# Kernel tuning notes

Measured on AMD Instinct MI355X. Metric: run time of the kernel, lower is better.

The kernel has to match this reference:

```python
import jax, jax.numpy as jnp
import numpy as np
from jax import lax

B, C1, C2, OUT, H, W = 8, 256, 128, 256, 64, 64
MID = max(C1, C2)
D = max(MID // 8, 4)

def conv1x1(x, w, b=None):
    # x: [B,C,H,W], w: [O,C]
    y = jnp.einsum('bchw,oc->bohw', x, w)
    if b is not None:
        y = y + b[None, :, None, None]
    return y

def dwconv3x3(x, w, b):
    # depthwise 3x3, padding=1; w: [C,1,3,3]
    y = lax.conv_general_dilated(x, w, (1, 1), 'SAME',
                                 dimension_numbers=('NCHW', 'OIHW', 'NCHW'),
                                 feature_group_count=x.shape[1])
    return y + b[None, :, None, None]

def setup_inputs() -> dict:
    key = jax.random.key(0)
    ks = jax.random.split(key, 16)
    def w1x1(k, o, i):
        return jax.random.normal(k, (o, i), jnp.float32) * np.sqrt(2.0 / o)
    def wdw(k, c):
        return jax.random.normal(k, (c, 1, 3, 3), jnp.float32) * np.sqrt(2.0 / (9 * c))
    z = lambda c: jnp.zeros((c,), jnp.float32)
    return {
        'x1': jax.random.normal(ks[0], (B, C1, H, W), jnp.float32),
        'x2': jax.random.normal(ks[1], (B, C2, H, W), jnp.float32),
        'conv_r_w': w1x1(ks[2], MID, C1), 'conv_r_b': z(MID),
        'conv_n_w': w1x1(ks[3], MID, C2), 'conv_n_b': z(MID),
        'mlp_w1': w1x1(ks[4], D, MID),
        'mlp_w2': w1x1(ks[5], 2 * MID, D),
        'pq_w': w1x1(ks[6], MID, MID), 'pq_b': z(MID),
        'dq_w': wdw(ks[7], MID), 'dq_b': z(MID),
        'pk_w': w1x1(ks[8], MID, MID), 'pk_b': z(MID),
        'dk_w': wdw(ks[9], MID), 'dk_b': z(MID),
        'pv_w': w1x1(ks[10], MID, MID), 'pv_b': z(MID),
        'dv_w': wdw(ks[11], MID), 'dv_b': z(MID),
        'out_w': w1x1(ks[12], OUT, MID), 'out_b': z(OUT),
        'alpha': jnp.float32(1.0),
        'lambd': jnp.float32(0.5),
        'beta': jnp.float32(0.5),
    }

def reference(x1, x2, conv_r_w, conv_r_b, conv_n_w, conv_n_b, mlp_w1, mlp_w2,
              pq_w, pq_b, dq_w, dq_b, pk_w, pk_b, dk_w, dk_b,
              pv_w, pv_b, dv_w, dv_b, out_w, out_b, alpha, lambd, beta):
    FR = conv1x1(x1, conv_r_w, conv_r_b)          # [B,C,H,W]
    FN = conv1x1(x2, conv_n_w, conv_n_b)          # [B,C,H,W]
    stack = jnp.stack([FR, FN], axis=1)           # [B,2,C,H,W]
    feats_sum = FR + FN
    pooled = feats_sum.mean(axis=(2, 3))          # [B,C] (adaptive avg pool 1x1)
    h = jax.nn.relu(jnp.einsum('bc,dc->bd', pooled, mlp_w1))
    a = jnp.einsum('bd,ed->be', h, mlp_w2).reshape(B, 2, MID)
    attn = jax.nn.softmax(a, axis=1)              # softmax over the 2 branches
    Fw = jnp.einsum('bkchw,bkc->bchw', stack, attn)
    Q = dwconv3x3(conv1x1(Fw, pq_w, pq_b), dq_w, dq_b)
    K = dwconv3x3(conv1x1(Fw, pk_w, pk_b), dk_w, dk_b)
    V = dwconv3x3(conv1x1(Fw, pv_w, pv_b), dv_w, dv_b)
    FQ = jnp.fft.fft2(Q.astype(jnp.float32), axes=(-2, -1))   # complex64 [B,C,H,W]
    FK = jnp.fft.fft2(K.astype(jnp.float32), axes=(-2, -1))
    elem = (FQ * FK).reshape(B, MID, H * W)                    # [B,C,HW]
    FQf = FQ.reshape(B, MID, H * W)
    FKf = FK.reshape(B, MID, H * W)
    attn_matrix = jnp.einsum('bcn,bdn->bcd', FQf, FKf)         # complex [B,C,C]
    attn_w = jax.nn.softmax(jnp.abs(attn_matrix) / alpha, axis=-1)
    attn_wc = attn_w.astype(jnp.complex64)
    F_CFR = jnp.einsum('bcd,bdn->bcn', attn_wc, elem).reshape(B, MID, H, W)
    cfr = jnp.real(jnp.fft.ifft2(F_CFR, axes=(-2, -1))).astype(Q.dtype)
    F_DFR = V - lambd * V * cfr
    freq_out = Q * cfr + F_DFR
    output = beta * freq_out + (1.0 - beta) * Fw
    return conv1x1(output, out_w, out_b)
```

## Files before the change

### kernel.cpp

```cpp
#include <hip/hip_runtime.h>
#include <math.h>

#ifndef M_PI
#define M_PI 3.14159265358979323846
#endif

typedef unsigned int u32;

constexpr int  NB   = 8;
constexpr int  CH   = 256;
constexpr long HW   = 4096;
constexpr long SLOT = (long)NB * CH * HW;
constexpr int  SPLITK = 8;
constexpr long ST   = (long)CH * HW;

__device__ __forceinline__ float rne_hi(float x) {
  unsigned u = __float_as_uint(x);
  unsigned r = (u + 0x7FFFu + ((u >> 16) & 1u)) & 0xFFFF0000u;
  return __uint_as_float(r);
}
__device__ __forceinline__ u32 packf(float x) {
  const float h = rne_hi(x);
  const float l = x - h;
  return (__float_as_uint(h) & 0xFFFF0000u) | (__float_as_uint(l) >> 16);
}
__device__ __forceinline__ float unpackf(u32 u) {
  return __uint_as_float(u & 0xFFFF0000u) + __uint_as_float(u << 16);
}
__device__ __forceinline__ unsigned bfpair(float x, float y) {
  return (__float_as_uint(x) >> 16) | (__float_as_uint(y) & 0xFFFF0000u);
}

typedef short bf16x8 __attribute__((ext_vector_type(8)));
typedef float f32x4  __attribute__((ext_vector_type(4)));

struct CvtJob { const float* src; u32* dst; int n4; };

__global__ __launch_bounds__(256)
void cvt_kernel(CvtJob j0, CvtJob j1, CvtJob j2, CvtJob j3, CvtJob j4, CvtJob j5)
{
  const int yy = blockIdx.y;
  CvtJob j;
  switch (yy) {
    case 0: j = j0; break;
    case 1: j = j1; break;
    case 2: j = j2; break;
    case 3: j = j3; break;
    case 4: j = j4; break;
    default: j = j5; break;
  }
  const int i = blockIdx.x * 256 + threadIdx.x;
  if (i < j.n4) {
    const float4 v = ((const float4*)j.src)[i];
    uint4 o;
    o.x = packf(v.x); o.y = packf(v.y); o.z = packf(v.z); o.w = packf(v.w);
    ((uint4*)j.dst)[i] = o;
  }
}

struct GemmSet {
  const u32*   A;
  const void*  B;
  void*        C;
  const float* bias;
  int          K;
  long         bStride;
};

#define SWZ(row, chunk) (((row) << 5) + ((((chunk) ^ ((row) & 3))) << 3))

template<bool BPACKED, int EPI>
__global__ __launch_bounds__(512, 2)
void gemm_mfma(GemmSet g0, GemmSet g1, GemmSet g2,
               long aStride, long cStride,
               const u32* __restrict__ qb, const u32* __restrict__ vb,
               const u32* __restrict__ fwb,
               const float* __restrict__ lambd, const float* __restrict__ beta)
{
  constexpr int N = 4096;
  __shared__ __align__(16) unsigned short sAh[256 * 32];
  __shared__ __align__(16) unsigned short sAl[256 * 32];
  __shared__ __align__(16) unsigned short sBh[128 * 32];
  __shared__ __align__(16) unsigned short sBl[128 * 32];

  const int tid = threadIdx.x;
  const int b   = blockIdx.z;
  const int yy  = blockIdx.y;
  const int n0  = blockIdx.x * 128;

  const GemmSet g = (yy == 0) ? g0 : ((yy == 1) ? g1 : g2);
  const u32*   A       = g.A;
  const void*  Bv      = g.B;
  void*        Cv      = g.C;
  const float* bias    = g.bias;
  const int    K       = g.K;
  const long   bStride = g.bStride;

  const u32* Ab = A + (long)b * aStride;

  const int ar = tid >> 1;
  const int ak = (tid & 1) * 16;
  const int ac0 = (tid & 1) * 2;
  const int bn = tid & 127;
  const int bc0 = tid >> 7;
  const int bk = bc0 * 8;

  const int wv = tid >> 6, lane = tid & 63;
  const int wy = wv >> 1, wx = wv & 1;
  const int quad = lane >> 4, l15 = lane & 15;

  f32x4 acc[4][4];
#pragma unroll
  for (int i = 0; i < 4; ++i)
#pragma unroll
    for (int j = 0; j < 4; ++j) acc[i][j] = (f32x4){0.f, 0.f, 0.f, 0.f};

  u32   ra[16];
  u32   rbu[8];
  float rbf[8];
  {
    const u32* ap = Ab + (long)ar * K + ak;
#pragma unroll
    for (int i = 0; i < 4; ++i) {
      const uint4 t = *(const uint4*)(ap + i * 4);
      ra[4*i] = t.x; ra[4*i+1] = t.y; ra[4*i+2] = t.z; ra[4*i+3] = t.w;
    }
    if (BPACKED) {
      const u32* bp = (const u32*)Bv + (long)b * bStride + (long)bk * N + n0 + bn;
#pragma unroll
      for (int i = 0; i < 8; ++i) rbu[i] = bp[(long)i * N];
    } else {
      const float* bp = (const float*)Bv + (long)b * bStride + (long)bk * N + n0 + bn;
#pragma unroll
      for (int i = 0; i < 8; ++i) rbf[i] = bp[(long)i * N];
    }
  }

  for (int kt = 0; kt < K; kt += 32) {
    {
      u32 hi[8], lo[8];
#pragma unroll
      for (int e = 0; e < 8; ++e) {
        const u32 u0 = ra[2*e], u1 = ra[2*e+1];
        hi[e] = (u0 >> 16) | (u1 & 0xFFFF0000u);
        lo[e] = (u0 & 0xFFFFu) | (u1 << 16);
      }
      *(uint4*)&sAh[SWZ(ar, ac0)]     = make_uint4(hi[0], hi[1], hi[2], hi[3]);
      *(uint4*)&sAh[SWZ(ar, ac0 + 1)] = make_uint4(hi[4], hi[5], hi[6], hi[7]);
      *(uint4*)&sAl[SWZ(ar, ac0)]     = make_uint4(lo[0], lo[1], lo[2], lo[3]);
      *(uint4*)&sAl[SWZ(ar, ac0 + 1)] = make_uint4(lo[4], lo[5], lo[6], lo[7]);
    }
    if (BPACKED) {
      u32 hi[4], lo[4];
#pragma unroll
      for (int e = 0; e < 4; ++e) {
        const u32 u0 = rbu[2*e], u1 = rbu[2*e+1];
        hi[e] = (u0 >> 16) | (u1 & 0xFFFF0000u);
        lo[e] = (u0 & 0xFFFFu) | (u1 << 16);
      }
      *(uint4*)&sBh[SWZ(bn, bc0)] = make_uint4(hi[0], hi[1], hi[2], hi[3]);
      *(uint4*)&sBl[SWZ(bn, bc0)] = make_uint4(lo[0], lo[1], lo[2], lo[3]);
    } else {
      float h[8], l[8];
#pragma unroll
      for (int e = 0; e < 8; ++e) { h[e] = rne_hi(rbf[e]); l[e] = rbf[e] - h[e]; }
      *(uint4*)&sBh[SWZ(bn, bc0)] = make_uint4(bfpair(h[0],h[1]), bfpair(h[2],h[3]),
                                               bfpair(h[4],h[5]), bfpair(h[6],h[7]));
      *(uint4*)&sBl[SWZ(bn, bc0)] = make_uint4(bfpair(l[0],l[1]), bfpair(l[2],l[3]),
                                               bfpair(l[4],l[5]), bfpair(l[6],l[7]));
    }
    __syncthreads();

    if (kt + 32 < K) {
      const u32* ap = Ab + (long)ar * K + kt + 32 + ak;
#pragma unroll
      for (int i = 0; i < 4; ++i) {
        const uint4 t = *(const uint4*)(ap + i * 4);
        ra[4*i] = t.x; ra[4*i+1] = t.y; ra[4*i+2] = t.z; ra[4*i+3] = t.w;
      }
      if (BPACKED) {
        const u32* bp = (const u32*)Bv + (long)b * bStride + (long)(kt + 32 + bk) * N + n0 + bn;
#pragma unroll
        for (int i = 0; i < 8; ++i) rbu[i] = bp[(long)i * N];
      } else {
        const float* bp = (const float*)Bv + (long)b * bStride + (long)(kt + 32 + bk) * N + n0 + bn;
#pragma unroll
        for (int i = 0; i < 8; ++i) rbf[i] = bp[(long)i * N];
      }
    }

    bf16x8 ah[4], al[4];
#pragma unroll
    for (int i = 0; i < 4; ++i) {
      const int rowa = wy * 64 + i * 16 + l15;
      ah[i] = *(const bf16x8*)&sAh[SWZ(rowa, quad)];
      al[i] = *(const bf16x8*)&sAl[SWZ(rowa, quad)];
    }
#pragma unroll
    for (int j = 0; j < 4; ++j) {
      const int rowb = wx * 64 + j * 16 + l15;
      const bf16x8 bh = *(const bf16x8*)&sBh[SWZ(rowb, quad)];
      const bf16x8 bl = *(const bf16x8*)&sBl[SWZ(rowb, quad)];
#pragma unroll
      for (int i = 0; i < 4; ++i) {
        acc[i][j] = __builtin_amdgcn_mfma_f32_16x16x32_bf16(ah[i], bh, acc[i][j], 0, 0, 0);
        acc[i][j] = __builtin_amdgcn_mfma_f32_16x16x32_bf16(ah[i], bl, acc[i][j], 0, 0, 0);
        acc[i][j] = __builtin_amdgcn_mfma_f32_16x16x32_bf16(al[i], bh, acc[i][j], 0, 0, 0);
      }
    }
    __syncthreads();
  }

  if (EPI == 0) {
    float* Cb = (float*)Cv + (long)b * cStride;
#pragma unroll
    for (int i = 0; i < 4; ++i)
#pragma unroll
      for (int r = 0; r < 4; ++r) {
        const int row = wy * 64 + i * 16 + quad * 4 + r;
        const float bb = bias ? bias[row] : 0.f;
#pragma unroll
        for (int j = 0; j < 4; ++j) {
          const int col = n0 + wx * 64 + j * 16 + l15;
          Cb[(long)row * N + col] = acc[i][j][r] + bb;
        }
      }
  } else if (EPI == 1) {
    u32* Cb = (u32*)Cv + (long)b * cStride;
#pragma unroll
    for (int i = 0; i < 4; ++i)
#pragma unroll
      for (int r = 0; r < 4; ++r) {
        const int row = wy * 64 + i * 16 + quad * 4 + r;
        const float bb = bias ? bias[row] : 0.f;
#pragma unroll
        for (int j = 0; j < 4; ++j) {
          const int col = n0 + wx * 64 + j * 16 + l15;
          Cb[(long)row * N + col] = packf(acc[i][j][r] + bb);
        }
      }
  } else {
    u32* Cb = (u32*)Cv + (long)b * cStride;
    const float lam = lambd[0], bet = beta[0];
#pragma unroll
    for (int i = 0; i < 4; ++i)
#pragma unroll
      for (int r = 0; r < 4; ++r) {
        const int row = wy * 64 + i * 16 + quad * 4 + r;
#pragma unroll
        for (int j = 0; j < 4; ++j) {
          const int col = n0 + wx * 64 + j * 16 + l15;
          const long off = (long)row * N + col;
          const long gi  = (long)b * cStride + off;
          const float q = unpackf(qb[gi]);
          const float v = unpackf(vb[gi]);
          const float f = unpackf(fwb[gi]);
          Cb[off] = packf(bet * (acc[i][j][r] * (q - lam * v) + v) + (1.f - bet) * f);
        }
      }
  }
}

__global__ __launch_bounds__(256)
void gemm_logits(const u32* __restrict__ Q, const u32* __restrict__ Kr,
                 float* __restrict__ Lp)
{
  __shared__ __align__(16) unsigned short sAh[128 * 48];
  __shared__ __align__(16) unsigned short sAl[128 * 48];
  __shared__ __align__(16) unsigned short sBh[128 * 48];
  __shared__ __align__(16) unsigned short sBl[128 * 48];

  const int tid = threadIdx.x;
  const int bz  = blockIdx.z;
  const int b   = bz >> 3, sp = bz & 7;
  const int m0  = blockIdx.y * 128;
  const int n0  = blockIdx.x * 128;
  const long k0b = (long)sp * 512;

  const int ar = tid >> 1;
  const int ak = (tid & 1) * 16;
  const int aBase = ar * 48 + ak;

  const int wv = tid >> 6, lane = tid & 63;
  const int wy = wv >> 1, wx = wv & 1;
  const int quad = lane >> 4, l15 = lane & 15;

  f32x4 acc[4][4];
#pragma unroll
  for (int i = 0; i < 4; ++i)
#pragma unroll
    for (int j = 0; j < 4; ++j) acc[i][j] = (f32x4){0.f, 0.f, 0.f, 0.f};

  const u32* Abase = Q  + (long)b * ST + (long)(m0 + ar) * 4096 + k0b + ak;
  const u32* Bbase = Kr + (long)b * ST + (long)(n0 + ar) * 4096 + k0b + ak;

  u32 ra[16], rb[16];
#pragma unroll
  for (int i = 0; i < 4; ++i) {
    uint4 t = *(const uint4*)(Abase + i * 4);
    ra[4*i] = t.x; ra[4*i+1] = t.y; ra[4*i+2] = t.z; ra[4*i+3] = t.w;
    t = *(const uint4*)(Bbase + i * 4);
    rb[4*i] = t.x; rb[4*i+1] = t.y; rb[4*i+2] = t.z; rb[4*i+3] = t.w;
  }

  for (int kt = 0; kt < 512; kt += 32) {
    {
      u32 hi[8], lo[8];
#pragma unroll
      for (int e = 0; e < 8; ++e) {
        const u32 u0 = ra[2*e], u1 = ra[2*e+1];
        hi[e] = (u0 >> 16) | (u1 & 0xFFFF0000u);
        lo[e] = (u0 & 0xFFFFu) | (u1 << 16);
      }
      *(uint4*)&sAh[aBase]     = make_uint4(hi[0], hi[1], hi[2], hi[3]);
      *(uint4*)&sAh[aBase + 8] = make_uint4(hi[4], hi[5], hi[6], hi[7]);
      *(uint4*)&sAl[aBase]     = make_uint4(lo[0], lo[1], lo[2], lo[3]);
      *(uint4*)&sAl[aBase + 8] = make_uint4(lo[4], lo[5], lo[6], lo[7]);
#pragma unroll
      for (int e = 0; e < 8; ++e) {
        const u32 u0 = rb[2*e], u1 = rb[2*e+1];
        hi[e] = (u0 >> 16) | (u1 & 0xFFFF0000u);
        lo[e] = (u0 & 0xFFFFu) | (u1 << 16);
      }
      *(uint4*)&sBh[aBase]     = make_uint4(hi[0], hi[1], hi[2], hi[3]);
      *(uint4*)&sBh[aBase + 8] = make_uint4(hi[4], hi[5], hi[6], hi[7]);
      *(uint4*)&sBl[aBase]     = make_uint4(lo[0], lo[1], lo[2], lo[3]);
      *(uint4*)&sBl[aBase + 8] = make_uint4(lo[4], lo[5], lo[6], lo[7]);
    }
    __syncthreads();

    if (kt + 32 < 512) {
#pragma unroll
      for (int i = 0; i < 4; ++i) {
        uint4 t = *(const uint4*)(Abase + kt + 32 + i * 4);
        ra[4*i] = t.x; ra[4*i+1] = t.y; ra[4*i+2] = t.z; ra[4*i+3] = t.w;
        t = *(const uint4*)(Bbase + kt + 32 + i * 4);
        rb[4*i] = t.x; rb[4*i+1] = t.y; rb[4*i+2] = t.z; rb[4*i+3] = t.w;
      }
    }

    bf16x8 ah[4], al[4];
#pragma unroll
    for (int i = 0; i < 4; ++i) {
      const int idx = (wy * 64 + i * 16 + l15) * 48 + quad * 8;
      ah[i] = *(const bf16x8*)&sAh[idx];
      al[i] = *(const bf16x8*)&sAl[idx];
    }
#pragma unroll
    for (int j = 0; j < 4; ++j) {
      const int idx = (wx * 64 + j * 16 + l15) * 48 + quad * 8;
      const bf16x8 bh = *(const bf16x8*)&sBh[idx];
      const bf16x8 bl = *(const bf16x8*)&sBl[idx];
#pragma unroll
      for (int i = 0; i < 4; ++i) {
        acc[i][j] = __builtin_amdgcn_mfma_f32_16x16x32_bf16(ah[i], bh, acc[i][j], 0, 0, 0);
        acc[i][j] = __builtin_amdgcn_mfma_f32_16x16x32_bf16(ah[i], bl, acc[i][j], 0, 0, 0);
        acc[i][j] = __builtin_amdgcn_mfma_f32_16x16x32_bf16(al[i], bh, acc[i][j], 0, 0, 0);
      }
    }
    __syncthreads();
  }

  float* Lb = Lp + (long)bz * 65536;
#pragma unroll
  for (int i = 0; i < 4; ++i)
#pragma unroll
    for (int r = 0; r < 4; ++r) {
      const int row = m0 + wy * 64 + i * 16 + quad * 4 + r;
#pragma unroll
      for (int j = 0; j < 4; ++j) {
        const int col = n0 + wx * 64 + j * 16 + l15;
        Lb[(long)row * 256 + col] = acc[i][j][r];
      }
    }
}

__global__ __launch_bounds__(256)
void pool_kernel(const u32* __restrict__ FR, const u32* __restrict__ FN,
                 float* __restrict__ pooled)
{
  __shared__ float red[256];
  const int bc = blockIdx.x, tid = threadIdx.x;
  const uint4* a = (const uint4*)(FR + (long)bc * HW);
  const uint4* b = (const uint4*)(FN + (long)bc * HW);
  float s = 0.f;
  for (int v = tid; v < 1024; v += 256) {
    const uint4 x = a[v];
    s += unpackf(x.x) + unpackf(x.y) + unpackf(x.z) + unpackf(x.w);
    const uint4 y = b[v];
    s += unpackf(y.x) + unpackf(y.y) + unpackf(y.z) + unpackf(y.w);
  }
  red[tid] = s; __syncthreads();
  for (int o = 128; o > 0; o >>= 1) {
    if (tid < o) red[tid] += red[tid + o];
    __syncthreads();
  }
  if (tid == 0) pooled[bc] = red[0] * (1.f / 4096.f);
}

__global__ __launch_bounds__(256)
void attn2_kernel(const float* __restrict__ pooled, const float* __restrict__ w1,
                  const float* __restrict__ w2, float* __restrict__ attn2)
{
  __shared__ float ps[256];
  __shared__ float hs[32];
  const int b = blockIdx.x, tid = threadIdx.x;
  ps[tid] = pooled[b * 256 + tid];
  __syncthreads();
  if (tid < 32) {
    float a = 0.f;
    for (int c = 0; c < 256; ++c) a += ps[c] * w1[tid * 256 + c];
    hs[tid] = fmaxf(a, 0.f);
  }
  __syncthreads();
  float a0 = 0.f, a1 = 0.f;
  for (int d = 0; d < 32; ++d) {
    const float h = hs[d];
    a0 += h * w2[tid * 32 + d];
    a1 += h * w2[(256 + tid) * 32 + d];
  }
  const float m  = fmaxf(a0, a1);
  const float e0 = expf(a0 - m), e1 = expf(a1 - m);
  const float inv = 1.f / (e0 + e1);
  attn2[b * 512 + tid]       = e0 * inv;
  attn2[b * 512 + 256 + tid] = e1 * inv;
}

__global__ __launch_bounds__(256)
void fw_kernel(const u32* __restrict__ FR, const u32* __restrict__ FN,
               const float* __restrict__ attn2, u32* __restrict__ FW)
{
  const int b = blockIdx.z, c = blockIdx.y;
  const float a0 = attn2[b * 512 + c];
  const float a1 = attn2[b * 512 + 256 + c];
  const long base4 = ((long)b * 256 + c) * 1024;
  const int i = blockIdx.x * 256 + threadIdx.x;
  const uint4 r = ((const uint4*)FR)[base4 + i];
  const uint4 n = ((const uint4*)FN)[base4 + i];
  uint4 o;
  o.x = packf(a0 * unpackf(r.x) + a1 * unpackf(n.x));
  o.y = packf(a0 * unpackf(r.y) + a1 * unpackf(n.y));
  o.z = packf(a0 * unpackf(r.z) + a1 * unpackf(n.z));
  o.w = packf(a0 * unpackf(r.w) + a1 * unpackf(n.w));
  ((uint4*)FW)[base4 + i] = o;
}

struct DwJob { const u32* in; const float* w; const float* bias; u32* out; u32* out_rev; };

__global__ __launch_bounds__(256)
void dw_kernel(DwJob j0, DwJob j1, DwJob j2)
{
  __shared__ float img[66][66];
  const int yy = blockIdx.y;
  const DwJob j = (yy == 0) ? j0 : ((yy == 1) ? j1 : j2);
  const int bc = blockIdx.x, tid = threadIdx.x;
  const int c = bc & 255;
  for (int v = tid; v < 66 * 66; v += 256) ((float*)img)[v] = 0.f;
  __syncthreads();
  const uint4* in4 = (const uint4*)(j.in + (long)bc * HW);
  for (int v = tid; v < 1024; v += 256) {
    const uint4 x = in4[v];
    const int r = v >> 4, c0 = ((v & 15) << 2) + 1;
    img[r + 1][c0 + 0] = unpackf(x.x);
    img[r + 1][c0 + 1] = unpackf(x.y);
    img[r + 1][c0 + 2] = unpackf(x.z);
    img[r + 1][c0 + 3] = unpackf(x.w);
  }
  float wr[9];
#pragma unroll
  for (int jj = 0; jj < 9; ++jj) wr[jj] = j.w[c * 9 + jj];
  const float bb = j.bias[c];
  __syncthreads();
  for (int p = tid; p < 4096; p += 256) {
    const int y = p >> 6, x = p & 63;
    float s = bb;
#pragma unroll
    for (int ky = 0; ky < 3; ++ky)
#pragma unroll
      for (int kx = 0; kx < 3; ++kx)
        s = fmaf(wr[ky * 3 + kx], img[y + ky][x + kx], s);
    const u32 u = packf(s);
    j.out[(long)bc * HW + p] = u;
    if (j.out_rev)
      j.out_rev[(long)bc * HW + (((64 - y) & 63) << 6) + ((64 - x) & 63)] = u;
  }
}

#define SWA(r, c) (((r) << 6) | ((c) ^ (r)))
#define REV6(x)   ((((x) & 3) << 4) | ((x) & 12) | ((x) >> 4))

__device__ __forceinline__ float2 cmul(float2 a, float2 w) {
  return make_float2(a.x * w.x - a.y * w.y, a.x * w.y + a.y * w.x);
}
__device__ __forceinline__ float2 cmulc(float2 a, float2 w) {
  return make_float2(a.x * w.x + a.y * w.y, a.y * w.x - a.x * w.y);
}
__device__ __forceinline__ void r4fwd(float2& x0, float2& x1, float2& x2, float2& x3) {
  const float2 t0 = make_float2(x0.x + x2.x, x0.y + x2.y);
  const float2 t1 = make_float2(x0.x - x2.x, x0.y - x2.y);
  const float2 t2 = make_float2(x1.x + x3.x, x1.y + x3.y);
  const float2 t3 = make_float2(x1.x - x3.x, x1.y - x3.y);
  x0 = make_float2(t0.x + t2.x, t0.y + t2.y);
  x2 = make_float2(t0.x - t2.x, t0.y - t2.y);
  x1 = make_float2(t1.x + t3.y, t1.y - t3.x);
  x3 = make_float2(t1.x - t3.y, t1.y + t3.x);
}
__device__ __forceinline__ void r4inv(float2& x0, float2& x1, float2& x2, float2& x3) {
  const float2 t0 = make_float2(x0.x + x2.x, x0.y + x2.y);
  const float2 t1 = make_float2(x0.x - x2.x, x0.y - x2.y);
  const float2 t2 = make_float2(x1.x + x3.x, x1.y + x3.y);
  const float2 t3 = make_float2(x1.x - x3.x, x1.y - x3.y);
  x0 = make_float2(t0.x + t2.x, t0.y + t2.y);
  x2 = make_float2(t0.x - t2.x, t0.y - t2.y);
  x1 = make_float2(t1.x - t3.y, t1.y + t3.x);
  x3 = make_float2(t1.x + t3.y, t1.y - t3.x);
}

__device__ __forceinline__ void fused01_fwd(float2* __restrict__ Z,
                                            const float2 (&wA)[3][3],
                                            int lane, int kb, int pass)
{
  float2 x[16];
#pragma unroll
  for (int m = 0; m < 16; ++m) {
    const int p = 16 * kb + m;
    x[m] = Z[pass ? SWA(p, lane) : SWA(lane, p)];
  }
#pragma unroll
  for (int c = 0; c < 4; ++c)
    r4fwd(x[4*c], x[4*c+1], x[4*c+2], x[4*c+3]);
#pragma unroll
  for (int j = 0; j < 4; ++j) {
    if (j) {
      x[j+4]  = cmul(x[j+4],  wA[j-1][0]);
      x[j+8]  = cmul(x[j+8],  wA[j-1][1]);
      x[j+12] = cmul(x[j+12], wA[j-1][2]);
    }
    r4fwd(x[j], x[j+4], x[j+8], x[j+12]);
  }
#pragma unroll
  for (int m = 0; m < 16; ++m) {
    const int p = 16 * kb + m;
    Z[pass ? SWA(p, lane) : SWA(lane, p)] = x[m];
  }
}

__device__ __forceinline__ void stage2_fwd(float2* __restrict__ Z,
                                           const float2 (&wB)[4][3],
                                           int lane, int kb, int pass)
{
#pragma unroll
  for (int q = 0; q < 4; ++q) {
    const int k = kb + 4 * q;
    const int a0 = pass ? SWA(k,      lane) : SWA(lane, k);
    const int a1 = pass ? SWA(k + 16, lane) : SWA(lane, k + 16);
    const int a2 = pass ? SWA(k + 32, lane) : SWA(lane, k + 32);
    const int a3 = pass ? SWA(k + 48, lane) : SWA(lane, k + 48);
    float2 x0 = Z[a0], x1 = Z[a1], x2 = Z[a2], x3 = Z[a3];
    x1 = cmul(x1, wB[q][0]);
    x2 = cmul(x2, wB[q][1]);
    x3 = cmul(x3, wB[q][2]);
    r4fwd(x0, x1, x2, x3);
    Z[a0] = x0; Z[a1] = x1; Z[a2] = x2; Z[a3] = x3;
  }
}

__device__ __forceinline__ void stage2_inv(float2* __restrict__ Z,
                                           const float2 (&wB)[4][3],
                                           int lane, int kb, int pass)
{
#pragma unroll
  for (int q = 0; q < 4; ++q) {
    const int k = kb + 4 * q;
    const int a0 = pass ? SWA(lane, k)      : SWA(k,      lane);
    const int a1 = pass ? SWA(lane, k + 16) : SWA(k + 16, lane);
    const int a2 = pass ? SWA(lane, k + 32) : SWA(k + 32, lane);
    const int a3 = pass ? SWA(lane, k + 48) : SWA(k + 48, lane);
    float2 x0 = Z[a0], x1 = Z[a1], x2 = Z[a2], x3 = Z[a3];
    r4inv(x0, x1, x2, x3);
    x1 = cmulc(x1, wB[q][0]);
    x2 = cmulc(x2, wB[q][1]);
    x3 = cmulc(x3, wB[q][2]);
    Z[a0] = x0; Z[a1] = x1; Z[a2] = x2; Z[a3] = x3;
  }
}

__device__ __forceinline__ void fused01_inv(float2* __restrict__ Z,
                                            const float2 (&wA)[3][3],
                                            int lane, int kb, int pass)
{
  float2 x[16];
#pragma unroll
  for (int m = 0; m < 16; ++m) {
    const int p = 16 * kb + m;
    x[m] = Z[pass ? SWA(lane, p) : SWA(p, lane)];
  }
#pragma unroll
  for (int j = 0; j < 4; ++j) {
    r4inv(x[j], x[j+4], x[j+8], x[j+12]);
    if (j) {
      x[j+4]  = cmulc(x[j+4],  wA[j-1][0]);
      x[j+8]  = cmulc(x[j+8],  wA[j-1][1]);
      x[j+12] = cmulc(x[j+12], wA[j-1][2]);
    }
  }
#pragma unroll
  for (int c = 0; c < 4; ++c)
    r4inv(x[4*c], x[4*c+1], x[4*c+2], x[4*c+3]);
#pragma unroll
  for (int m = 0; m < 16; ++m) {
    const int p = 16 * kb + m;
    Z[pass ? SWA(lane, p) : SWA(p, lane)] = x[m];
  }
}

__device__ __forceinline__ void sconv_load(float2* __restrict__ Z,
                                           const u32* __restrict__ Qg,
                                           const u32* __restrict__ Kg,
                                           long base, int tid)
{
  const uint4* Q4 = (const uint4*)(Qg + base);
  const uint4* K4 = (const uint4*)(Kg + base);
#pragma unroll
  for (int i = 0; i < 4; ++i) {
    const int v = tid + 256 * i;
    const uint4 q = Q4[v], k = K4[v];
    const int r = v >> 4, w = v & 15;
    const int R  = REV6(r);
    const int cb = ((w & 3) << 2) | (w >> 2);
    Z[SWA(R, cb)]      = make_float2(unpackf(q.x), unpackf(k.x));
    Z[SWA(R, cb + 16)] = make_float2(unpackf(q.y), unpackf(k.y));
    Z[SWA(R, cb + 32)] = make_float2(unpackf(q.z), unpackf(k.z));
    Z[SWA(R, cb + 48)] = make_float2(unpackf(q.w), unpackf(k.w));
  }
}

__global__ __launch_bounds__(256, 2)
void sconv_kernel(const u32* __restrict__ Qg, const u32* __restrict__ Kg,
                  u32* __restrict__ Sg)
{
  __shared__ float2 ZA[4096];
  __shared__ float2 ZB[4096];
  const int tid  = threadIdx.x;
  const int lane = tid & 63;
  const int kb   = tid >> 6;
  const long base = (long)blockIdx.x * 8192;

  const float2 wA[3][3] = {
    { make_float2( 0.92387953251f, -0.38268343236f),
      make_float2( 0.70710678119f, -0.70710678119f),
      make_float2( 0.38268343236f, -0.92387953251f) },
    { make_float2( 0.70710678119f, -0.70710678119f),
      make_float2( 0.f,            -1.f),
      make_float2(-0.70710678119f, -0.70710678119f) },
    { make_float2( 0.38268343236f, -0.92387953251f),
      make_float2(-0.70710678119f, -0.70710678119f),
      make_float2(-0.92387953251f,  0.38268343236f) } };
  float2 wB[4][3];
#pragma unroll
  for (int q = 0; q < 4; ++q) {
    const float k = (float)(kb + 4 * q);
    float sn, cs;
    __sincosf(-2.f * (float)M_PI * (1.f / 64.f) * k,        &sn, &cs); wB[q][0] = make_float2(cs, sn);
    __sincosf(-2.f * (float)M_PI * (1.f / 64.f) * (2.f*k),  &sn, &cs); wB[q][1] = make_float2(cs, sn);
    __sincosf(-2.f * (float)M_PI * (1.f / 64.f) * (3.f*k),  &sn, &cs); wB[q][2] = make_float2(cs, sn);
  }

  sconv_load(ZA, Qg, Kg, base, tid);
  sconv_load(ZB, Qg, Kg, base + 4096, tid);
  __syncthreads();

  for (int pass = 0; pass < 2; ++pass) {
    fused01_fwd(ZA, wA, lane, kb, pass);
    fused01_fwd(ZB, wA, lane, kb, pass);
    __syncthreads();
    stage2_fwd(ZA, wB, lane, kb, pass);
    stage2_fwd(ZB, wB, lane, kb, pass);
    __syncthreads();
  }

#pragma unroll
  for (int i = 0; i < 9; ++i) {
    const int n = tid + 256 * i;
    if (n < 2112) {
      const int u = n >> 6, vv = n & 63;
      if (!((u == 0 || u == 32) && vv > 32)) {
        const int u2 = (64 - u) & 63, v2 = (64 - vv) & 63;
        const int az = SWA(u, vv), am = SWA(u2, v2);
        const float2 z0 = ZA[az], m0 = ZA[am];
        const float2 z1 = ZB[az], m1 = ZB[am];
        const float dre0 = 0.25f * (z0.x*z0.x - z0.y*z0.y - m0.x*m0.x + m0.y*m0.y);
        const float dim0 = 0.5f  * (z0.x*z0.y + m0.x*m0.y);
        const float dre1 = 0.25f * (z1.x*z1.x - z1.y*z1.y - m1.x*m1.x + m1.y*m1.y);
        const float dim1 = 0.5f  * (z1.x*z1.y + m1.x*m1.y);
        ZA[az] = make_float2(dim0 + dre1, dim1 - dre0);
        ZA[am] = make_float2(dim0 - dre1, dim1 + dre0);
      }
    }
  }
  __syncthreads();

  for (int pass = 0; pass < 2; ++pass) {
    stage2_inv(ZA, wB, lane, kb, pass);
    __syncthreads();
    fused01_inv(ZA, wA, lane, kb, pass);
    __syncthreads();
  }

  uint4* Sa = (uint4*)(Sg + base);
  uint4* Sb = (uint4*)(Sg + base + 4096);
#pragma unroll
  for (int i = 0; i < 4; ++i) {
    const int v = tid + 256 * i;
    const int y = v >> 4, w = v & 15;
    const int Rr = REV6(y);
    const int cb = ((w & 3) << 2) | (w >> 2);
    const float2 e0 = ZA[SWA(Rr, cb)];
    const float2 e1 = ZA[SWA(Rr, cb + 16)];
    const float2 e2 = ZA[SWA(Rr, cb + 32)];
    const float2 e3 = ZA[SWA(Rr, cb + 48)];
    uint4 o;
    o.x = packf(e0.x * (1.f / 4096.f));
    o.y = packf(e1.x * (1.f / 4096.f));
    o.z = packf(e2.x * (1.f / 4096.f));
    o.w = packf(e3.x * (1.f / 4096.f));
    Sa[v] = o;
    o.x = packf(e0.y * (1.f / 4096.f));
    o.y = packf(e1.y * (1.f / 4096.f));
    o.z = packf(e2.y * (1.f / 4096.f));
    o.w = packf(e3.y * (1.f / 4096.f));
    Sb[v] = o;
  }
}

__global__ __launch_bounds__(256)
void softmax_kernel(const float* __restrict__ Lp, u32* __restrict__ L,
                    const float* __restrict__ alpha)
{
  __shared__ float red[256];
  const int row = blockIdx.x, tid = threadIdx.x;
  const int b = row >> 8, c = row & 255;
  const float sc = 4096.f / alpha[0];
  float acc = 0.f;
#pragma unroll
  for (int s = 0; s < SPLITK; ++s)
    acc += Lp[((long)(b * SPLITK + s) * 65536) + (long)c * 256 + tid];
  const float v = fabsf(acc) * sc;
  red[tid] = v; __syncthreads();
  for (int o = 128; o > 0; o >>= 1) {
    if (tid < o) red[tid] = fmaxf(red[tid], red[tid + o]);
    __syncthreads();
  }
  const float mx = red[0];
  __syncthreads();
  const float e = expf(v - mx);
  red[tid] = e; __syncthreads();
  for (int o = 128; o > 0; o >>= 1) {
    if (tid < o) red[tid] += red[tid + o];
    __syncthreads();
  }
  L[(long)row * 256 + tid] = packf(e / red[0]);
}

extern "C" void kernel_launch(void* const* d_in, const int* in_sizes, int n_in,
                              void* d_out, int out_size, void* d_ws, size_t ws_size,
                              hipStream_t stream)
{
  const float* x1       = (const float*)d_in[0];
  const float* x2       = (const float*)d_in[1];
  const float* conv_r_w = (const float*)d_in[2];
  const float* conv_r_b = (const float*)d_in[3];
  const float* conv_n_w = (const float*)d_in[4];
  const float* conv_n_b = (const float*)d_in[5];
  const float* mlp_w1   = (const float*)d_in[6];
  const float* mlp_w2   = (const float*)d_in[7];
  const float* pq_w     = (const float*)d_in[8];
  const float* pq_b     = (const float*)d_in[9];
  const float* dq_w     = (const float*)d_in[10];
  const float* dq_b     = (const float*)d_in[11];
  const float* pk_w     = (const float*)d_in[12];
  const float* pk_b     = (const float*)d_in[13];
  const float* dk_w     = (const float*)d_in[14];
  const float* dk_b     = (const float*)d_in[15];
  const float* pv_w     = (const float*)d_in[16];
  const float* pv_b     = (const float*)d_in[17];
  const float* dv_w     = (const float*)d_in[18];
  const float* dv_b     = (const float*)d_in[19];
  const float* out_w    = (const float*)d_in[20];
  const float* out_b    = (const float*)d_in[21];
  const float* alpha    = (const float*)d_in[22];
  const float* lambd    = (const float*)d_in[23];
  const float* beta     = (const float*)d_in[24];

  u32* s = (u32*)d_ws;
  u32* S0 = s;
  u32* S1 = s + SLOT;
  u32* S2 = s + 2 * SLOT;
  u32* S3 = s + 3 * SLOT;
  u32* S4 = s + 4 * SLOT;
  u32* S5 = s + 5 * SLOT;
  float* Lp     = (float*)(s + 6 * SLOT);
  u32*   Lb     = (u32*)(Lp + (long)8 * SPLITK * 65536);
  float* pooled = (float*)(Lb + (long)8 * 65536);
  float* attn2  = pooled + 2048;
  u32*   wR     = (u32*)(attn2 + 4096);
  u32*   wN     = wR + 65536;
  u32*   wQ     = wN + 32768;
  u32*   wK     = wQ + 65536;
  u32*   wV     = wK + 65536;
  u32*   wO     = wV + 65536;

  const size_t needed =
      (size_t)(6 * SLOT + (long)8 * SPLITK * 65536 + 8L * 65536 + 2048 + 4096
               + 65536 * 5 + 32768) * 4;
  if (ws_size < needed) return;

  const long ST2 = (long)128 * HW;
  const long STL = (long)256 * 256;

  {
    CvtJob jR{conv_r_w, wR, 16384};
    CvtJob jQ{pq_w,     wQ, 16384};
    CvtJob jK{pk_w,     wK, 16384};
    CvtJob jV{pv_w,     wV, 16384};
    CvtJob jO{out_w,    wO, 16384};
    CvtJob jN{conv_n_w, wN, 8192};
    cvt_kernel<<<dim3(64, 6), 256, 0, stream>>>(jR, jQ, jK, jV, jO, jN);
  }

  {
    GemmSet gR{wR, (const void*)x1, (void*)S0, conv_r_b, 256, ST};
    GemmSet gN{wN, (const void*)x2, (void*)S1, conv_n_b, 128, ST2};
    gemm_mfma<false, 1><<<dim3(32, 2, 8), 512, 0, stream>>>(gR, gN, gN,
        0L, ST, nullptr, nullptr, nullptr, nullptr, nullptr);
  }

  pool_kernel<<<2048, 256, 0, stream>>>(S0, S1, pooled);
  attn2_kernel<<<8, 256, 0, stream>>>(pooled, mlp_w1, mlp_w2, attn2);
  fw_kernel<<<dim3(4, 256, 8), 256, 0, stream>>>(S0, S1, attn2, S2);

  {
    GemmSet gQ{wQ, (const void*)S2, (void*)S3, pq_b, 256, ST};
    GemmSet gK{wK, (const void*)S2, (void*)S4, pk_b, 256, ST};
    GemmSet gV{wV, (const void*)S2, (void*)S5, pv_b, 256, ST};
    gemm_mfma<true, 1><<<dim3(32, 3, 8), 512, 0, stream>>>(gQ, gK, gV,
        0L, ST, nullptr, nullptr, nullptr, nullptr, nullptr);
  }

  {
    DwJob jQ{S3, dq_w, dq_b, S0, nullptr};
    DwJob jK{S4, dk_w, dk_b, S1, S3};
    DwJob jV{S5, dv_w, dv_b, S4, nullptr};
    dw_kernel<<<dim3(2048, 3), 256, 0, stream>>>(jQ, jK, jV);
  }

  sconv_kernel<<<1024, 256, 0, stream>>>(S0, S1, S5);

  gemm_logits<<<dim3(2, 2, 64), 256, 0, stream>>>(S0, S3, Lp);
  softmax_kernel<<<2048, 256, 0, stream>>>(Lp, Lb, alpha);

  {
    GemmSet gM{Lb, (const void*)S5, (void*)S2, nullptr, 256, ST};
    gemm_mfma<true, 2><<<dim3(32, 1, 8), 512, 0, stream>>>(gM, gM, gM,
        STL, ST, S0, S4, S2, lambd, beta);
  }

  {
    GemmSet gO{wO, (const void*)S2, d_out, out_b, 256, ST};
    gemm_mfma<true, 0><<<dim3(32, 1, 8), 512, 0, stream>>>(gO, gO, gO,
        0L, ST, nullptr, nullptr, nullptr, nullptr, nullptr);
  }
}
```

Baseline: 440.8 us.

## Double-buffer GEMM shared tiles with padded rows instead of XOR swizzle

Converts the MFMA GEMM's LDS staging to a two-buffer ping-pong so the next tile is committed after the MFMA work and only one barrier per k-step is needed. The XOR swizzle is replaced by a padded row stride of 48 elements. This raises LDS use to about 144KB per block, which likely drops residency to one block per CU despite the launch bound of two. The padding may also change bank-conflict behaviour.

```diff
diff --git a/kernel.cpp b/kernel.cpp
--- a/kernel.cpp
+++ b/kernel.cpp
@@ -67,7 +67,50 @@
   long         bStride;
 };
 
-#define SWZ(row, chunk) (((row) << 5) + ((((chunk) ^ ((row) & 3))) << 3))
+__device__ __forceinline__ void commitA48(unsigned short* __restrict__ dh,
+                                          unsigned short* __restrict__ dl,
+                                          const u32* ra, int aBase)
+{
+  u32 hi[8], lo[8];
+#pragma unroll
+  for (int e = 0; e < 8; ++e) {
+    const u32 u0 = ra[2*e], u1 = ra[2*e+1];
+    hi[e] = (u0 >> 16) | (u1 & 0xFFFF0000u);
+    lo[e] = (u0 & 0xFFFFu) | (u1 << 16);
+  }
+  *(uint4*)&dh[aBase]     = make_uint4(hi[0], hi[1], hi[2], hi[3]);
+  *(uint4*)&dh[aBase + 8] = make_uint4(hi[4], hi[5], hi[6], hi[7]);
+  *(uint4*)&dl[aBase]     = make_uint4(lo[0], lo[1], lo[2], lo[3]);
+  *(uint4*)&dl[aBase + 8] = make_uint4(lo[4], lo[5], lo[6], lo[7]);
+}
+
+__device__ __forceinline__ void commitBu48(unsigned short* __restrict__ dh,
+                                           unsigned short* __restrict__ dl,
+                                           const u32* rbu, int bBase)
+{
+  u32 hi[4], lo[4];
+#pragma unroll
+  for (int e = 0; e < 4; ++e) {
+    const u32 u0 = rbu[2*e], u1 = rbu[2*e+1];
+    hi[e] = (u0 >> 16) | (u1 & 0xFFFF0000u);
+    lo[e] = (u0 & 0xFFFFu) | (u1 << 16);
+  }
+  *(uint4*)&dh[bBase] = make_uint4(hi[0], hi[1], hi[2], hi[3]);
+  *(uint4*)&dl[bBase] = make_uint4(lo[0], lo[1], lo[2], lo[3]);
+}
+
+__device__ __forceinline__ void commitBf48(unsigned short* __restrict__ dh,
+                                           unsigned short* __restrict__ dl,
+                                           const float* rbf, int bBase)
+{
+  float h[8], l[8];
+#pragma unroll
+  for (int e = 0; e < 8; ++e) { h[e] = rne_hi(rbf[e]); l[e] = rbf[e] - h[e]; }
+  *(uint4*)&dh[bBase] = make_uint4(bfpair(h[0],h[1]), bfpair(h[2],h[3]),
+                                   bfpair(h[4],h[5]), bfpair(h[6],h[7]));
+  *(uint4*)&dl[bBase] = make_uint4(bfpair(l[0],l[1]), bfpair(l[2],l[3]),
+                                   bfpair(l[4],l[5]), bfpair(l[6],l[7]));
+}
 
 template<bool BPACKED, int EPI>
 __global__ __launch_bounds__(512, 2)
@@ -78,10 +121,10 @@
                const float* __restrict__ lambd, const float* __restrict__ beta)
 {
   constexpr int N = 4096;
-  __shared__ __align__(16) unsigned short sAh[256 * 32];
-  __shared__ __align__(16) unsigned short sAl[256 * 32];
-  __shared__ __align__(16) unsigned short sBh[128 * 32];
-  __shared__ __align__(16) unsigned short sBl[128 * 32];
+  __shared__ __align__(16) unsigned short sAh[2][256 * 48];
+  __shared__ __align__(16) unsigned short sAl[2][256 * 48];
+  __shared__ __align__(16) unsigned short sBh[2][128 * 48];
+  __shared__ __align__(16) unsigned short sBl[2][128 * 48];
 
   const int tid = threadIdx.x;
   const int b   = blockIdx.z;
@@ -100,10 +143,10 @@
 
   const int ar = tid >> 1;
   const int ak = (tid & 1) * 16;
-  const int ac0 = (tid & 1) * 2;
+  const int aBase = ar * 48 + ak;
   const int bn = tid & 127;
-  const int bc0 = tid >> 7;
-  const int bk = bc0 * 8;
+  const int bk = (tid >> 7) * 8;
+  const int bBase = bn * 48 + bk;
 
   const int wv = tid >> 6, lane = tid & 63;
   const int wy = wv >> 1, wx = wv & 1;
@@ -118,6 +161,7 @@
   u32   ra[16];
   u32   rbu[8];
   float rbf[8];
+
   {
     const u32* ap = Ab + (long)ar * K + ak;
 #pragma unroll
@@ -135,43 +179,16 @@
       for (int i = 0; i < 8; ++i) rbf[i] = bp[(long)i * N];
     }
   }
-
+  commitA48(sAh[0], sAl[0], ra, aBase);
+  if (BPACKED) commitBu48(sBh[0], sBl[0], rbu, bBase);
+  else         commitBf48(sBh[0], sBl[0], rbf, bBase);
+  __syncthreads();
+
+  int cur = 0;
   for (int kt = 0; kt < K; kt += 32) {
-    {
-      u32 hi[8], lo[8];
-#pragma unroll
-      for (int e = 0; e < 8; ++e) {
-        const u32 u0 = ra[2*e], u1 = ra[2*e+1];
-        hi[e] = (u0 >> 16) | (u1 & 0xFFFF0000u);
-        lo[e] = (u0 & 0xFFFFu) | (u1 << 16);
-      }
-      *(uint4*)&sAh[SWZ(ar, ac0)]     = make_uint4(hi[0], hi[1], hi[2], hi[3]);
-      *(uint4*)&sAh[SWZ(ar, ac0 + 1)] = make_uint4(hi[4], hi[5], hi[6], hi[7]);
-      *(uint4*)&sAl[SWZ(ar, ac0)]     = make_uint4(lo[0], lo[1], lo[2], lo[3]);
-      *(uint4*)&sAl[SWZ(ar, ac0 + 1)] = make_uint4(lo[4], lo[5], lo[6], lo[7]);
-    }
-    if (BPACKED) {
-      u32 hi[4], lo[4];
-#pragma unroll
-      for (int e = 0; e < 4; ++e) {
-        const u32 u0 = rbu[2*e], u1 = rbu[2*e+1];
-        hi[e] = (u0 >> 16) | (u1 & 0xFFFF0000u);
-        lo[e] = (u0 & 0xFFFFu) | (u1 << 16);
-      }
-      *(uint4*)&sBh[SWZ(bn, bc0)] = make_uint4(hi[0], hi[1], hi[2], hi[3]);
-      *(uint4*)&sBl[SWZ(bn, bc0)] = make_uint4(lo[0], lo[1], lo[2], lo[3]);
-    } else {
-      float h[8], l[8];
-#pragma unroll
-      for (int e = 0; e < 8; ++e) { h[e] = rne_hi(rbf[e]); l[e] = rbf[e] - h[e]; }
-      *(uint4*)&sBh[SWZ(bn, bc0)] = make_uint4(bfpair(h[0],h[1]), bfpair(h[2],h[3]),
-                                               bfpair(h[4],h[5]), bfpair(h[6],h[7]));
-      *(uint4*)&sBl[SWZ(bn, bc0)] = make_uint4(bfpair(l[0],l[1]), bfpair(l[2],l[3]),
-                                               bfpair(l[4],l[5]), bfpair(l[6],l[7]));
-    }
-    __syncthreads();
-
-    if (kt + 32 < K) {
+    const bool more = (kt + 32 < K);
+
+    if (more) {
       const u32* ap = Ab + (long)ar * K + kt + 32 + ak;
 #pragma unroll
       for (int i = 0; i < 4; ++i) {
@@ -189,26 +206,40 @@
       }
     }
 
-    bf16x8 ah[4], al[4];
-#pragma unroll
-    for (int i = 0; i < 4; ++i) {
-      const int rowa = wy * 64 + i * 16 + l15;
-      ah[i] = *(const bf16x8*)&sAh[SWZ(rowa, quad)];
-      al[i] = *(const bf16x8*)&sAl[SWZ(rowa, quad)];
-    }
-#pragma unroll
-    for (int j = 0; j < 4; ++j) {
-      const int rowb = wx * 64 + j * 16 + l15;
-      const bf16x8 bh = *(const bf16x8*)&sBh[SWZ(rowb, quad)];
-      const bf16x8 bl = *(const bf16x8*)&sBl[SWZ(rowb, quad)];
+    {
+      const unsigned short* cAh = sAh[cur];
+      const unsigned short* cAl = sAl[cur];
+      const unsigned short* cBh = sBh[cur];
+      const unsigned short* cBl = sBl[cur];
+      bf16x8 ah[4], al[4];
 #pragma unroll
       for (int i = 0; i < 4; ++i) {
-        acc[i][j] = __builtin_amdgcn_mfma_f32_16x16x32_bf16(ah[i], bh, acc[i][j], 0, 0, 0);
-        acc[i][j] = __builtin_amdgcn_mfma_f32_16x16x32_bf16(ah[i], bl, acc[i][j], 0, 0, 0);
-        acc[i][j] = __builtin_amdgcn_mfma_f32_16x16x32_bf16(al[i], bh, acc[i][j], 0, 0, 0);
-      }
+        const int idx = (wy * 64 + i * 16 + l15) * 48 + quad * 8;
+        ah[i] = *(const bf16x8*)&cAh[idx];
+        al[i] = *(const bf16x8*)&cAl[idx];
+      }
+#pragma unroll
+      for (int j = 0; j < 4; ++j) {
+        const int idx = (wx * 64 + j * 16 + l15) * 48 + quad * 8;
+        const bf16x8 bh = *(const bf16x8*)&cBh[idx];
+        const bf16x8 bl = *(const bf16x8*)&cBl[idx];
+#pragma unroll
+        for (int i = 0; i < 4; ++i) {
+          acc[i][j] = __builtin_amdgcn_mfma_f32_16x16x32_bf16(ah[i], bh, acc[i][j], 0, 0, 0);
+          acc[i][j] = __builtin_amdgcn_mfma_f32_16x16x32_bf16(ah[i], bl, acc[i][j], 0, 0, 0);
+          acc[i][j] = __builtin_amdgcn_mfma_f32_16x16x32_bf16(al[i], bh, acc[i][j], 0, 0, 0);
+        }
+      }
+    }
+
+    if (more) {
+      const int nb = cur ^ 1;
+      commitA48(sAh[nb], sAl[nb], ra, aBase);
+      if (BPACKED) commitBu48(sBh[nb], sBl[nb], rbu, bBase);
+      else         commitBf48(sBh[nb], sBl[nb], rbf, bBase);
     }
     __syncthreads();
+    if (more) cur ^= 1;
   }
 
   if (EPI == 0) {
```

Result: no change. 432.8 us (-1.8%).
